# Optimization experiments

Measured on AMD Instinct MI355X. Metric: run time of the kernel, lower is better.

Reference implementation:

```python
import jax, jax.numpy as jnp
import numpy as np

B, T, D, H, E, M = 4, 2048, 2048, 8, 512, 8  # batch, seq, hidden, moe_heads, moe_experts, moe_dim//2
F = E * M  # flatten_shape = 4096
HALF = D // 2


def act(z):
    # 'relu2' activation: relu(x)**2
    r = jax.nn.relu(z)
    return r * r


def setup_inputs() -> dict:
    key = jax.random.key(0)
    ks = jax.random.split(key, 13)
    s = 0.02
    return {
        "x": jax.random.normal(ks[0], (B, T, D), jnp.float32),
        "g1": jax.random.uniform(ks[1], (B, T, H, E), jnp.float32),
        "g2": jax.random.uniform(ks[2], (B, T, H, E), jnp.float32),
        "u1_w": jax.random.normal(ks[3], (F, D), jnp.float32) * s,
        "u1_b": jnp.zeros((F,), jnp.float32),
        "u2_w": jax.random.normal(ks[4], (F, D), jnp.float32) * s,
        "u2_b": jnp.zeros((F,), jnp.float32),
        "v11_w": jax.random.normal(ks[5], (HALF, F), jnp.float32) * s,
        "v12_w": jax.random.normal(ks[6], (HALF, F), jnp.float32) * s,
        "v21_w": jax.random.normal(ks[7], (HALF, F), jnp.float32) * s,
        "v22_w": jax.random.normal(ks[8], (HALF, F), jnp.float32) * s,
        "b1": jax.random.normal(ks[9], (E, HALF), jnp.float32) * s,
        "b2": jax.random.normal(ks[10], (E, HALF), jnp.float32) * s,
    }


def reference(x, g1, g2, u1_w, u1_b, u2_w, u2_b, v11_w, v12_w, v21_w, v22_w, b1, b2):
    # x1, x2: [B,T,E,M]
    x1 = act(x @ u1_w.T + u1_b).reshape(B, T, E, M)
    x2 = act(x @ u2_w.T + u2_b).reshape(B, T, E, M)

    g1s = g1.sum(axis=2)  # [B,T,E] (einsum '...hi->...i')
    g2s = g2.sum(axis=2)

    # x11 = v11(einsum('btim,bthi->btim', x1, g1).flatten(-2))
    x11 = (x1 * g1s[..., None]).reshape(B, T, F) @ v11_w.T
    # x12 = v12(einsum('btjm,bthj,bthi->btim', x2, g2, g1).flatten(-2))
    t2 = jnp.einsum('btjm,bthj->bthm', x2, g2)
    x12 = jnp.einsum('bthm,bthi->btim', t2, g1).reshape(B, T, F) @ v12_w.T
    # x13 = einsum('bthi,id->btd', g1, b1)
    x13 = g1s @ b1

    # x21 = v21(einsum('btim,bthi,bthj->btjm', x1, g1, g2).flatten(-2))
    t1 = jnp.einsum('btim,bthi->bthm', x1, g1)
    x21 = jnp.einsum('bthm,bthj->btjm', t1, g2).reshape(B, T, F) @ v21_w.T
    # x22 = v22(einsum('btjm,bthj->btjm', x2, g2).flatten(-2))
    x22 = (x2 * g2s[..., None]).reshape(B, T, F) @ v22_w.T
    # x23 = einsum('bthj,jd->btd', g2, b2)
    x23 = g2s @ b2

    return jnp.concatenate((x11 + x12 + x13, x21 + x22 + x23), axis=-1)
```

## Files before the change

kernel.cpp:

```cpp
#include <hip/hip_runtime.h>
#include <hip/hip_bf16.h>

#define TOK   8192
#define DD    2048
#define FF    4096
#define EE    512
#define HALF  1024
#define KCAT  8704

typedef __bf16 bf16x8 __attribute__((ext_vector_type(8)));
typedef __bf16 bf16x4 __attribute__((ext_vector_type(4)));
typedef float  f32x4  __attribute__((ext_vector_type(4)));
using bf16 = __hip_bfloat16;

#define AS1(p) ((const __attribute__((address_space(1))) void*)(p))
#define AS3(p) ((__attribute__((address_space(3))) void*)(p))


__global__ void cvt_bf16(const float* __restrict__ in, bf16* __restrict__ out, int n4) {
    int i = blockIdx.x * blockDim.x + threadIdx.x;
    int stride = gridDim.x * blockDim.x;
    for (; i < n4; i += stride) {
        float4 v = ((const float4*)in)[i];
        bf16x4 o;
        o[0] = (__bf16)v.x; o[1] = (__bf16)v.y; o[2] = (__bf16)v.z; o[3] = (__bf16)v.w;
        ((bf16x4*)out)[i] = o;
    }
}

__global__ void pack_w(const float* __restrict__ vA, const float* __restrict__ vB,
                       const float* __restrict__ bmat, bf16* __restrict__ W) {
    int n = blockIdx.x;
    const float* ra = vA + (size_t)n * FF;
    const float* rb = vB + (size_t)n * FF;
    bf16* w = W + (size_t)n * KCAT;
    for (int k = threadIdx.x; k < FF; k += 256) {
        w[k]      = __float2bfloat16(ra[k]);
        w[FF + k] = __float2bfloat16(rb[k]);
    }
    for (int e = threadIdx.x; e < EE; e += 256)
        w[2 * FF + e] = __float2bfloat16(bmat[(size_t)e * HALF + n]);
}

template<int MODE>
__global__ __launch_bounds__(512, 2)
void gemm8(const bf16* __restrict__ A0, const bf16* __restrict__ B0,
           const float* __restrict__ bias0, void* __restrict__ C0,
           const bf16* __restrict__ A1, const bf16* __restrict__ B1,
           const float* __restrict__ bias1, void* __restrict__ C1,
           int nbm, int nbn, int K, int ldc)
{
    __shared__ __align__(16) char smem[3 * 32768];
    const int tid  = threadIdx.x;
    const int lane = tid & 63;
    const int wid  = tid >> 6;
    const int wm = wid >> 2, wn = wid & 3;
    const int r16 = lane & 15, kb = lane >> 4;

    int bid = blockIdx.x;
    {
        int nwg = gridDim.x;
        int q = nwg >> 3, r = nwg & 7;
        int xcd = bid & 7, idx = bid >> 3;
        bid = (xcd < r ? xcd * (q + 1) : r * (q + 1) + (xcd - r) * q) + idx;
    }
    const int npg = nbm * nbn;
    const int g   = bid / npg;
    const int lb  = bid - g * npg;
    const int bm = lb / nbn, bn = lb - bm * nbn;

    const bf16*  A    = g ? A1 : A0;
    const bf16*  Bw   = g ? B1 : B0;
    const float* bias = g ? bias1 : bias0;
    char* Cout = (char*)(g ? C1 : C0);

    const long row0 = (long)bm * 256;
    const int  col0 = bn * 256;
    const int  nt   = K >> 5;

    const char* gp[4];
    uint32_t ldst[4];
    #pragma unroll
    for (int l = 0; l < 4; ++l) {
        const int ab = l >> 1;
        const int li = l & 1;
        const uint32_t S = (uint32_t)(li * 512 + tid) * 16;
        const uint32_t L = S ^ (((S >> 7) & 3) << 4);
        const int r  = (int)(L >> 6);
        const int c2 = (int)(L & 63);
        const bf16* src = ab ? (Bw + (long)(col0 + r) * K) : (A + (row0 + r) * (long)K);
        gp[l]   = (const char*)src + c2;
        ldst[l] = (uint32_t)(ab * 16384) + (uint32_t)((li * 512 + (tid & ~63)) * 16);
    }

    uint32_t aoff, boff;
    {   int R0 = wm * 128 + r16;
        aoff = (uint32_t)((R0 * 64 + kb * 16) ^ (((R0 >> 1) & 3) << 4)); }
    {   int S0 = wn * 64 + r16;
        boff = 16384u + (uint32_t)((S0 * 64 + kb * 16) ^ (((S0 >> 1) & 3) << 4)); }

    f32x4 acc[8][4];
    #pragma unroll
    for (int i = 0; i < 8; ++i)
        #pragma unroll
        for (int j = 0; j < 4; ++j)
            acc[i][j] = (f32x4){0.f, 0.f, 0.f, 0.f};

    #pragma unroll
    for (int tt = 0; tt < 2; ++tt)
        #pragma unroll
        for (int l = 0; l < 4; ++l)
            __builtin_amdgcn_global_load_lds(AS1(gp[l] + tt * 64),
                                             AS3(smem + tt * 32768 + ldst[l]), 16, 0, 0);
    #pragma unroll
    for (int l = 0; l < 4; ++l) gp[l] += 128;

    int buf = 0;
    for (int t = 0; t < nt; ++t) {
        int sb = buf + 2; if (sb >= 3) sb -= 3;
        if (t + 2 < nt) {
            #pragma unroll
            for (int l = 0; l < 4; ++l) {
                __builtin_amdgcn_global_load_lds(AS1(gp[l]),
                                                 AS3(smem + sb * 32768 + ldst[l]), 16, 0, 0);
                gp[l] += 64;
            }
            asm volatile("s_waitcnt vmcnt(8)\n\ts_barrier" ::: "memory");
        } else if (t + 2 == nt) {
            asm volatile("s_waitcnt vmcnt(4)\n\ts_barrier" ::: "memory");
        } else {
            asm volatile("s_waitcnt vmcnt(0)\n\ts_barrier" ::: "memory");
        }

        const char* pb = smem + buf * 32768;
        bf16x8 af[8], bv[4];
        #pragma unroll
        for (int i = 0; i < 8; ++i)
            af[i] = *(const bf16x8*)(pb + aoff + i * 1024);
        #pragma unroll
        for (int j = 0; j < 4; ++j)
            bv[j] = *(const bf16x8*)(pb + boff + j * 1024);

        __builtin_amdgcn_s_setprio(1);
        #pragma unroll
        for (int i = 0; i < 8; ++i)
            #pragma unroll
            for (int j = 0; j < 4; ++j)
                acc[i][j] = __builtin_amdgcn_mfma_f32_16x16x32_bf16(af[i], bv[j], acc[i][j], 0, 0, 0);
        __builtin_amdgcn_s_setprio(0);

        asm volatile("s_barrier" ::: "memory");
        buf = (buf == 2) ? 0 : buf + 1;
    }

    const int rb = (lane >> 4) * 4;
    #pragma unroll
    for (int i = 0; i < 8; ++i) {
        #pragma unroll
        for (int j = 0; j < 4; ++j) {
            const int cc = col0 + wn * 64 + j * 16 + r16;
            float badd = 0.f;
            if (MODE == 1) badd = bias[cc];
            #pragma unroll
            for (int e = 0; e < 4; ++e) {
                long row = row0 + wm * 128 + i * 16 + rb + e;
                float v = acc[i][j][e];
                if (MODE == 1) {
                    v += badd;
                    v = fmaxf(v, 0.f);
                    v = v * v;
                    ((bf16*)Cout)[row * ldc + cc] = __float2bfloat16(v);
                } else {
                    ((float*)Cout)[row * ldc + cc] = v;
                }
            }
        }
    }
}

#define GPAD 524
__global__ __launch_bounds__(256)
void glue(const float* __restrict__ g1, const float* __restrict__ g2,
          bf16* __restrict__ Yl, bf16* __restrict__ Yr)
{
    __shared__ __align__(16) float g1t[8 * GPAD];
    __shared__ __align__(16) float g2t[8 * GPAD];
    __shared__ float g1s[EE], g2s[EE];
    __shared__ float t1s[64], t2s[64];
    __shared__ float t1p[4][64], t2p[4][64];
    __shared__ __align__(16) bf16 x1t[FF], x2t[FF];

    const int t   = blockIdx.x;
    const int tid = threadIdx.x;
    const float* g1p = g1 + (size_t)t * FF;
    const float* g2p = g2 + (size_t)t * FF;
    bf16* ylp = Yl + (size_t)t * KCAT;
    bf16* yrp = Yr + (size_t)t * KCAT;

    #pragma unroll
    for (int c = 0; c < 4; ++c) {
        int idx4 = (c * 256 + tid) * 4;
        float4 v1 = *(const float4*)(g1p + idx4);
        float4 v2 = *(const float4*)(g2p + idx4);
        int h = idx4 >> 9, e = idx4 & 511;
        *(float4*)&g1t[h * GPAD + e] = v1;
        *(float4*)&g2t[h * GPAD + e] = v2;
    }
    #pragma unroll
    for (int c = 0; c < 2; ++c) {
        int idx8 = (c * 256 + tid) * 8;
        *(bf16x8*)&x1t[idx8] = *(const bf16x8*)(ylp + idx8);
        *(bf16x8*)&x2t[idx8] = *(const bf16x8*)(yrp + FF + idx8);
    }
    __syncthreads();

    #pragma unroll
    for (int c = 0; c < 2; ++c) {
        int e = c * 256 + tid;
        float s1 = 0.f, s2 = 0.f;
        #pragma unroll
        for (int h = 0; h < 8; ++h) { s1 += g1t[h * GPAD + e]; s2 += g2t[h * GPAD + e]; }
        g1s[e] = s1; g2s[e] = s2;
    }

    {
        int o = tid & 63;
        int h = o & 7, m = o >> 3;
        int p = tid >> 6;
        float s1 = 0.f, s2 = 0.f;
        #pragma unroll 8
        for (int ii = 0; ii < 128; ++ii) {
            int e = p * 128 + ii;
            float xv1 = __bfloat162float(x1t[e * 8 + m]);
            float xv2 = __bfloat162float(x2t[e * 8 + m]);
            s1 += xv1 * g1t[h * GPAD + e];
            s2 += xv2 * g2t[h * GPAD + e];
        }
        t1p[p][o] = s1; t2p[p][o] = s2;
    }
    __syncthreads();
    if (tid < 64)       t1s[tid] = t1p[0][tid] + t1p[1][tid] + t1p[2][tid] + t1p[3][tid];
    else if (tid < 128) { int o = tid - 64; t2s[o] = t2p[0][o] + t2p[1][o] + t2p[2][o] + t2p[3][o]; }
    __syncthreads();

    #pragma unroll
    for (int c = 0; c < 2; ++c) {
        int f0 = (c * 256 + tid) * 8;
        int e  = f0 >> 3;
        float s1 = g1s[e], s2 = g2s[e];
        bf16x8 xa = *(const bf16x8*)&x1t[f0];
        bf16x8 xb = *(const bf16x8*)&x2t[f0];
        bf16x8 o1, o2;
        #pragma unroll
        for (int u = 0; u < 8; ++u) {
            o1[u] = (__bf16)((float)xa[u] * s1);
            o2[u] = (__bf16)((float)xb[u] * s2);
        }
        *(bf16x8*)(ylp + f0)      = o1;
        *(bf16x8*)(yrp + FF + f0) = o2;
    }
    #pragma unroll
    for (int c = 0; c < 2; ++c) {
        int f0 = (c * 256 + tid) * 8;
        int i  = f0 >> 3;
        bf16x8 o12v, o21v;
        #pragma unroll
        for (int m = 0; m < 8; ++m) {
            float s12 = 0.f, s21 = 0.f;
            #pragma unroll
            for (int h = 0; h < 8; ++h) {
                s12 += t2s[(m << 3) | h] * g1t[h * GPAD + i];
                s21 += t1s[(m << 3) | h] * g2t[h * GPAD + i];
            }
            o12v[m] = (__bf16)s12;
            o21v[m] = (__bf16)s21;
        }
        *(bf16x8*)(ylp + FF + f0) = o12v;
        *(bf16x8*)(yrp + f0)      = o21v;
    }
    {
        int e0 = tid * 2;
        ylp[2 * FF + e0]     = __float2bfloat16(g1s[e0]);
        ylp[2 * FF + e0 + 1] = __float2bfloat16(g1s[e0 + 1]);
        yrp[2 * FF + e0]     = __float2bfloat16(g2s[e0]);
        yrp[2 * FF + e0 + 1] = __float2bfloat16(g2s[e0 + 1]);
    }
}


extern "C" void kernel_launch(void* const* d_in, const int* in_sizes, int n_in,
                              void* d_out, int out_size, void* d_ws, size_t ws_size,
                              hipStream_t stream) {
    const float* x    = (const float*)d_in[0];
    const float* g1   = (const float*)d_in[1];
    const float* g2   = (const float*)d_in[2];
    const float* u1_w = (const float*)d_in[3];
    const float* u1_b = (const float*)d_in[4];
    const float* u2_w = (const float*)d_in[5];
    const float* u2_b = (const float*)d_in[6];
    const float* v11  = (const float*)d_in[7];
    const float* v12  = (const float*)d_in[8];
    const float* v21  = (const float*)d_in[9];
    const float* v22  = (const float*)d_in[10];
    const float* b1   = (const float*)d_in[11];
    const float* b2   = (const float*)d_in[12];
    float* out = (float*)d_out;

    size_t off = 0;
    char* base = (char*)d_ws;
    auto take = [&](size_t bytes) { void* p = base + off; off += (bytes + 255) & ~(size_t)255; return p; };
    bf16* Xb  = (bf16*)take((size_t)TOK * DD * 2);
    bf16* U1b = (bf16*)take((size_t)FF * DD * 2);
    bf16* U2b = (bf16*)take((size_t)FF * DD * 2);
    bf16* Wl  = (bf16*)take((size_t)HALF * KCAT * 2);
    bf16* Wr  = (bf16*)take((size_t)HALF * KCAT * 2);
    bf16* Yl  = (bf16*)take((size_t)TOK * KCAT * 2);
    bf16* Yr  = (bf16*)take((size_t)TOK * KCAT * 2);

    cvt_bf16<<<4096, 256, 0, stream>>>(x,    Xb,  TOK * DD / 4);
    cvt_bf16<<<2048, 256, 0, stream>>>(u1_w, U1b, FF * DD / 4);
    cvt_bf16<<<2048, 256, 0, stream>>>(u2_w, U2b, FF * DD / 4);
    pack_w<<<HALF, 256, 0, stream>>>(v11, v12, b1, Wl);
    pack_w<<<HALF, 256, 0, stream>>>(v21, v22, b2, Wr);

    gemm8<1><<<2 * (TOK / 256) * (FF / 256), 512, 0, stream>>>(
        Xb, U1b, u1_b, Yl,
        Xb, U2b, u2_b, Yr + FF,
        TOK / 256, FF / 256, DD, KCAT);

    glue<<<TOK, 256, 0, stream>>>(g1, g2, Yl, Yr);

    gemm8<0><<<2 * (TOK / 256) * (HALF / 256), 512, 0, stream>>>(
        Yl, Wl, nullptr, out,
        Yr, Wr, nullptr, out + HALF,
        TOK / 256, HALF / 256, KCAT, DD);
}
```

Baseline: 750.4 us.

## Rewrite GEMM mainloop with 32x32x16 MFMA and phased double-buffered 64-wide K tiles

Replaces the 16x16x32 MFMA GEMM with one that uses 32x32x16 MFMA tiles, a K step of 64 split into four phases, and a two-stage 128KB LDS double buffer. Global-to-LDS loads for the next tile are interleaved with the LDS reads and MFMAs of each phase, and the XOR swizzle is changed to match. The larger MFMA shape needs fewer LDS fragment reads per FLOP, and finer-grained phases are meant to hide load latency better. The cost is more barriers per iteration and 128KB of LDS per block, which may limit occupancy to one block per CU despite the launch bound of two.

Measured after the change: 831.0 us. +10.7%, slower.

```diff
diff --git a/kernel.cpp b/kernel.cpp
--- a/kernel.cpp
+++ b/kernel.cpp
@@ -11,6 +11,7 @@
 typedef __bf16 bf16x8 __attribute__((ext_vector_type(8)));
 typedef __bf16 bf16x4 __attribute__((ext_vector_type(4)));
 typedef float  f32x4  __attribute__((ext_vector_type(4)));
+typedef float  f32x16 __attribute__((ext_vector_type(16)));
 using bf16 = __hip_bfloat16;
 
 #define AS1(p) ((const __attribute__((address_space(1))) void*)(p))
@@ -44,18 +45,18 @@
 
 template<int MODE>
 __global__ __launch_bounds__(512, 2)
-void gemm8(const bf16* __restrict__ A0, const bf16* __restrict__ B0,
-           const float* __restrict__ bias0, void* __restrict__ C0,
-           const bf16* __restrict__ A1, const bf16* __restrict__ B1,
-           const float* __restrict__ bias1, void* __restrict__ C1,
-           int nbm, int nbn, int K, int ldc)
+void gemm32(const bf16* __restrict__ A0, const bf16* __restrict__ B0,
+            const float* __restrict__ bias0, void* __restrict__ C0,
+            const bf16* __restrict__ A1, const bf16* __restrict__ B1,
+            const float* __restrict__ bias1, void* __restrict__ C1,
+            int nbm, int nbn, int K, int ldc)
 {
-    __shared__ __align__(16) char smem[3 * 32768];
+    __shared__ __align__(16) char smem[131072];
     const int tid  = threadIdx.x;
     const int lane = tid & 63;
     const int wid  = tid >> 6;
     const int wm = wid >> 2, wn = wid & 3;
-    const int r16 = lane & 15, kb = lane >> 4;
+    const int ln31 = lane & 31, kb = lane >> 5;
 
     int bid = blockIdx.x;
     {
@@ -76,95 +77,110 @@
 
     const long row0 = (long)bm * 256;
     const int  col0 = bn * 256;
-    const int  nt   = K >> 5;
-
-    const char* gp[4];
-    uint32_t ldst[4];
-    #pragma unroll
-    for (int l = 0; l < 4; ++l) {
-        const int ab = l >> 1;
-        const int li = l & 1;
-        const uint32_t S = (uint32_t)(li * 512 + tid) * 16;
-        const uint32_t L = S ^ (((S >> 7) & 3) << 4);
-        const int r  = (int)(L >> 6);
-        const int c2 = (int)(L & 63);
-        const bf16* src = ab ? (Bw + (long)(col0 + r) * K) : (A + (row0 + r) * (long)K);
-        gp[l]   = (const char*)src + c2;
-        ldst[l] = (uint32_t)(ab * 16384) + (uint32_t)((li * 512 + (tid & ~63)) * 16);
-    }
-
-    uint32_t aoff, boff;
-    {   int R0 = wm * 128 + r16;
-        aoff = (uint32_t)((R0 * 64 + kb * 16) ^ (((R0 >> 1) & 3) << 4)); }
-    {   int S0 = wn * 64 + r16;
-        boff = 16384u + (uint32_t)((S0 * 64 + kb * 16) ^ (((S0 >> 1) & 3) << 4)); }
-
-    f32x4 acc[8][4];
-    #pragma unroll
-    for (int i = 0; i < 8; ++i)
-        #pragma unroll
-        for (int j = 0; j < 4; ++j)
-            acc[i][j] = (f32x4){0.f, 0.f, 0.f, 0.f};
-
-    #pragma unroll
-    for (int tt = 0; tt < 2; ++tt)
-        #pragma unroll
-        for (int l = 0; l < 4; ++l)
-            __builtin_amdgcn_global_load_lds(AS1(gp[l] + tt * 64),
-                                             AS3(smem + tt * 32768 + ldst[l]), 16, 0, 0);
-    #pragma unroll
-    for (int l = 0; l < 4; ++l) gp[l] += 128;
-
-    int buf = 0;
+    const int  nt   = K >> 6;
+
+    const char* gA[2]; const char* gB[2];
+    uint32_t ldst0, ldst1;
+    #pragma unroll
+    for (int l = 0; l < 2; ++l) {
+        const uint32_t S = (uint32_t)(l * 512 + tid) * 16;
+        const int r  = (int)(S >> 6);
+        const int cb = (int)((S & 63) ^ ((uint32_t)(r & 3) << 4));
+        gA[l] = (const char*)A + (row0 + r) * (long)K * 2 + cb;
+        gB[l] = (const char*)Bw + (long)(col0 + r) * K * 2 + cb;
+    }
+    ldst0 = (uint32_t)(tid & ~63) * 16;
+    ldst1 = 8192u + (uint32_t)(tid & ~63) * 16;
+
+    const uint32_t aB = (uint32_t)(wm * 128 + ln31) * 64;
+    const uint32_t bB = 32768u + (uint32_t)(wn * 64 + ln31) * 64;
+    const uint32_t coffE = (uint32_t)((kb ^ (lane & 3)) << 4);
+    const uint32_t coffO = (uint32_t)(((kb | 2) ^ (lane & 3)) << 4);
+
+    f32x16 acc[4][2];
+    #pragma unroll
+    for (int i = 0; i < 4; ++i)
+        #pragma unroll
+        for (int j = 0; j < 2; ++j)
+            acc[i][j] = (f32x16)(0.f);
+
+    __builtin_amdgcn_global_load_lds(AS1(gA[0]),      AS3(smem +     0 + ldst0), 16, 0, 0);
+    __builtin_amdgcn_global_load_lds(AS1(gA[1]),      AS3(smem +     0 + ldst1), 16, 0, 0);
+    __builtin_amdgcn_global_load_lds(AS1(gB[0]),      AS3(smem + 32768 + ldst0), 16, 0, 0);
+    __builtin_amdgcn_global_load_lds(AS1(gB[1]),      AS3(smem + 32768 + ldst1), 16, 0, 0);
+    __builtin_amdgcn_global_load_lds(AS1(gA[0] + 64), AS3(smem + 16384 + ldst0), 16, 0, 0);
+    __builtin_amdgcn_global_load_lds(AS1(gA[1] + 64), AS3(smem + 16384 + ldst1), 16, 0, 0);
+    __builtin_amdgcn_global_load_lds(AS1(gB[0] + 64), AS3(smem + 49152 + ldst0), 16, 0, 0);
+    __builtin_amdgcn_global_load_lds(AS1(gB[1] + 64), AS3(smem + 49152 + ldst1), 16, 0, 0);
+    asm volatile("s_waitcnt vmcnt(4)\n\ts_barrier" ::: "memory");
+
+#define MFMA8()                                                                        \
+    __builtin_amdgcn_s_setprio(1);                                                     \
+    acc[0][0] = __builtin_amdgcn_mfma_f32_32x32x16_bf16(a0, b0, acc[0][0], 0, 0, 0);   \
+    acc[0][1] = __builtin_amdgcn_mfma_f32_32x32x16_bf16(a0, b1, acc[0][1], 0, 0, 0);   \
+    acc[1][0] = __builtin_amdgcn_mfma_f32_32x32x16_bf16(a1, b0, acc[1][0], 0, 0, 0);   \
+    acc[1][1] = __builtin_amdgcn_mfma_f32_32x32x16_bf16(a1, b1, acc[1][1], 0, 0, 0);   \
+    acc[2][0] = __builtin_amdgcn_mfma_f32_32x32x16_bf16(a2, b0, acc[2][0], 0, 0, 0);   \
+    acc[2][1] = __builtin_amdgcn_mfma_f32_32x32x16_bf16(a2, b1, acc[2][1], 0, 0, 0);   \
+    acc[3][0] = __builtin_amdgcn_mfma_f32_32x32x16_bf16(a3, b0, acc[3][0], 0, 0, 0);   \
+    acc[3][1] = __builtin_amdgcn_mfma_f32_32x32x16_bf16(a3, b1, acc[3][1], 0, 0, 0);   \
+    __builtin_amdgcn_s_setprio(0);
+
+#define PHASE(Q, LOFF, COFFv)                                                          \
+    {                                                                                  \
+        if (st) {                                                                      \
+            __builtin_amdgcn_global_load_lds(                                          \
+                AS1(((Q & 1) ? gB : gA)[0] + koff + (Q >> 1) * 64),                    \
+                AS3(pt + LOFF + ldst0), 16, 0, 0);                                     \
+            __builtin_amdgcn_global_load_lds(                                          \
+                AS1(((Q & 1) ? gB : gA)[1] + koff + (Q >> 1) * 64),                    \
+                AS3(pt + LOFF + ldst1), 16, 0, 0);                                     \
+        }                                                                              \
+        const char* ps = pb + (Q >> 1) * 16384;                                        \
+        bf16x8 a0 = *(const bf16x8*)(ps + aB + COFFv);                                 \
+        bf16x8 a1 = *(const bf16x8*)(ps + aB + 2048 + COFFv);                          \
+        bf16x8 a2 = *(const bf16x8*)(ps + aB + 4096 + COFFv);                          \
+        bf16x8 a3 = *(const bf16x8*)(ps + aB + 6144 + COFFv);                          \
+        bf16x8 b0 = *(const bf16x8*)(ps + bB + COFFv);                                 \
+        bf16x8 b1 = *(const bf16x8*)(ps + bB + 2048 + COFFv);                          \
+        asm volatile("s_barrier" ::: "memory");                                        \
+        MFMA8();                                                                       \
+    }
+
     for (int t = 0; t < nt; ++t) {
-        int sb = buf + 2; if (sb >= 3) sb -= 3;
-        if (t + 2 < nt) {
-            #pragma unroll
-            for (int l = 0; l < 4; ++l) {
-                __builtin_amdgcn_global_load_lds(AS1(gp[l]),
-                                                 AS3(smem + sb * 32768 + ldst[l]), 16, 0, 0);
-                gp[l] += 64;
-            }
-            asm volatile("s_waitcnt vmcnt(8)\n\ts_barrier" ::: "memory");
-        } else if (t + 2 == nt) {
-            asm volatile("s_waitcnt vmcnt(4)\n\ts_barrier" ::: "memory");
-        } else {
-            asm volatile("s_waitcnt vmcnt(0)\n\ts_barrier" ::: "memory");
-        }
-
-        const char* pb = smem + buf * 32768;
-        bf16x8 af[8], bv[4];
-        #pragma unroll
-        for (int i = 0; i < 8; ++i)
-            af[i] = *(const bf16x8*)(pb + aoff + i * 1024);
-        #pragma unroll
-        for (int j = 0; j < 4; ++j)
-            bv[j] = *(const bf16x8*)(pb + boff + j * 1024);
-
-        __builtin_amdgcn_s_setprio(1);
-        #pragma unroll
-        for (int i = 0; i < 8; ++i)
-            #pragma unroll
-            for (int j = 0; j < 4; ++j)
-                acc[i][j] = __builtin_amdgcn_mfma_f32_16x16x32_bf16(af[i], bv[j], acc[i][j], 0, 0, 0);
-        __builtin_amdgcn_s_setprio(0);
-
+        char* pb = smem + (t & 1) * 65536;
+        char* pt = smem + ((t + 1) & 1) * 65536;
+        const bool st = (t + 1 < nt);
+        const long koff = (long)(t + 1) * 128;
+
+        PHASE(0, 0, coffE)
         asm volatile("s_barrier" ::: "memory");
-        buf = (buf == 2) ? 0 : buf + 1;
-    }
-
-    const int rb = (lane >> 4) * 4;
-    #pragma unroll
-    for (int i = 0; i < 8; ++i) {
-        #pragma unroll
-        for (int j = 0; j < 4; ++j) {
-            const int cc = col0 + wn * 64 + j * 16 + r16;
+        PHASE(1, 32768, coffO)
+        if (st) asm volatile("s_waitcnt vmcnt(4)" ::: "memory");
+        else    asm volatile("s_waitcnt vmcnt(0)" ::: "memory");
+        asm volatile("s_barrier" ::: "memory");
+        PHASE(2, 16384, coffE)
+        asm volatile("s_barrier" ::: "memory");
+        PHASE(3, 49152, coffO)
+        if (st) asm volatile("s_waitcnt vmcnt(4)" ::: "memory");
+        asm volatile("s_barrier" ::: "memory");
+    }
+#undef PHASE
+#undef MFMA8
+
+    const int rowb = wm * 128 + kb * 4;
+    const int colb = col0 + wn * 64 + ln31;
+    #pragma unroll
+    for (int i = 0; i < 4; ++i) {
+        #pragma unroll
+        for (int j = 0; j < 2; ++j) {
+            const int cc = colb + j * 32;
             float badd = 0.f;
             if (MODE == 1) badd = bias[cc];
             #pragma unroll
-            for (int e = 0; e < 4; ++e) {
-                long row = row0 + wm * 128 + i * 16 + rb + e;
-                float v = acc[i][j][e];
+            for (int rg = 0; rg < 16; ++rg) {
+                long row = row0 + rowb + i * 32 + (rg & 3) + 8 * (rg >> 2);
+                float v = acc[i][j][rg];
                 if (MODE == 1) {
                     v += badd;
                     v = fmaxf(v, 0.f);
@@ -323,14 +339,14 @@
     pack_w<<<HALF, 256, 0, stream>>>(v11, v12, b1, Wl);
     pack_w<<<HALF, 256, 0, stream>>>(v21, v22, b2, Wr);
 
-    gemm8<1><<<2 * (TOK / 256) * (FF / 256), 512, 0, stream>>>(
+    gemm32<1><<<2 * (TOK / 256) * (FF / 256), 512, 0, stream>>>(
         Xb, U1b, u1_b, Yl,
         Xb, U2b, u2_b, Yr + FF,
         TOK / 256, FF / 256, DD, KCAT);
 
     glue<<<TOK, 256, 0, stream>>>(g1, g2, Yl, Yr);
 
-    gemm8<0><<<2 * (TOK / 256) * (HALF / 256), 512, 0, stream>>>(
+    gemm32<0><<<2 * (TOK / 256) * (HALF / 256), 512, 0, stream>>>(
         Yl, Wl, nullptr, out,
         Yr, Wr, nullptr, out + HALF,
         TOK / 256, HALF / 256, KCAT, DD);
```

## Restructure GEMM mainloop into ping-pong pipeline with K=64 tiles and split MFMA phases

Applied to the files above, without the earlier changes.

Replaces the triple-buffered K=32 mainloop with a double-buffered K=64 tile (128KB LDS) and splits each iteration into four MFMA phases. Each phase interleaves a quarter of the next tile's global-to-LDS loads with LDS fragment reads, separated by barriers. The intent is to overlap memory traffic with MFMA work at finer granularity and to cut per-tile loop overhead. The larger LDS footprint may allow only one 512-thread block per CU despite launch_bounds(512,2), and the extra barriers add synchronisation cost.

Result: faster. 714.4 us (-4.8%).

```diff
diff --git a/kernel.cpp b/kernel.cpp
--- a/kernel.cpp
+++ b/kernel.cpp
@@ -44,13 +44,13 @@
 
 template<int MODE>
 __global__ __launch_bounds__(512, 2)
-void gemm8(const bf16* __restrict__ A0, const bf16* __restrict__ B0,
+void gemmP(const bf16* __restrict__ A0, const bf16* __restrict__ B0,
            const float* __restrict__ bias0, void* __restrict__ C0,
            const bf16* __restrict__ A1, const bf16* __restrict__ B1,
            const float* __restrict__ bias1, void* __restrict__ C1,
            int nbm, int nbn, int K, int ldc)
 {
-    __shared__ __align__(16) char smem[3 * 32768];
+    __shared__ __align__(16) char smem[131072];
     const int tid  = threadIdx.x;
     const int lane = tid & 63;
     const int wid  = tid >> 6;
@@ -76,28 +76,22 @@
 
     const long row0 = (long)bm * 256;
     const int  col0 = bn * 256;
-    const int  nt   = K >> 5;
-
-    const char* gp[4];
-    uint32_t ldst[4];
-    #pragma unroll
-    for (int l = 0; l < 4; ++l) {
-        const int ab = l >> 1;
-        const int li = l & 1;
-        const uint32_t S = (uint32_t)(li * 512 + tid) * 16;
-        const uint32_t L = S ^ (((S >> 7) & 3) << 4);
-        const int r  = (int)(L >> 6);
-        const int c2 = (int)(L & 63);
-        const bf16* src = ab ? (Bw + (long)(col0 + r) * K) : (A + (row0 + r) * (long)K);
-        gp[l]   = (const char*)src + c2;
-        ldst[l] = (uint32_t)(ab * 16384) + (uint32_t)((li * 512 + (tid & ~63)) * 16);
-    }
-
-    uint32_t aoff, boff;
-    {   int R0 = wm * 128 + r16;
-        aoff = (uint32_t)((R0 * 64 + kb * 16) ^ (((R0 >> 1) & 3) << 4)); }
-    {   int S0 = wn * 64 + r16;
-        boff = 16384u + (uint32_t)((S0 * 64 + kb * 16) ^ (((S0 >> 1) & 3) << 4)); }
+    const int  nt   = K >> 6;
+
+    const char* gA[2]; const char* gB[2];
+    #pragma unroll
+    for (int l = 0; l < 2; ++l) {
+        const uint32_t S = (uint32_t)(l * 512 + tid) * 16;
+        const int r  = (int)(S >> 6);
+        const int cb = (int)((S & 63) ^ ((uint32_t)((r >> 1) & 3) << 4));
+        gA[l] = (const char*)A  + (row0 + r) * (long)K * 2 + cb;
+        gB[l] = (const char*)Bw + (long)(col0 + r) * K * 2 + cb;
+    }
+    const uint32_t ldst = (uint32_t)(tid & ~63) * 16;
+
+    const uint32_t swz  = ((uint32_t)(r16 >> 1) & 3u) << 4;
+    const uint32_t aoff = (uint32_t)((wm * 128 + r16) * 64 + kb * 16) ^ swz;
+    const uint32_t boff = (uint32_t)((wn * 64  + r16) * 64 + kb * 16) ^ swz;
 
     f32x4 acc[8][4];
     #pragma unroll
@@ -106,52 +100,84 @@
         for (int j = 0; j < 4; ++j)
             acc[i][j] = (f32x4){0.f, 0.f, 0.f, 0.f};
 
-    #pragma unroll
-    for (int tt = 0; tt < 2; ++tt)
-        #pragma unroll
-        for (int l = 0; l < 4; ++l)
-            __builtin_amdgcn_global_load_lds(AS1(gp[l] + tt * 64),
-                                             AS3(smem + tt * 32768 + ldst[l]), 16, 0, 0);
-    #pragma unroll
-    for (int l = 0; l < 4; ++l) gp[l] += 128;
-
-    int buf = 0;
+    __builtin_amdgcn_global_load_lds(AS1(gA[0]),      AS3(smem +     0 + ldst), 16, 0, 0);
+    __builtin_amdgcn_global_load_lds(AS1(gA[1]),      AS3(smem +  8192 + ldst), 16, 0, 0);
+    __builtin_amdgcn_global_load_lds(AS1(gB[0]),      AS3(smem + 32768 + ldst), 16, 0, 0);
+    __builtin_amdgcn_global_load_lds(AS1(gB[1]),      AS3(smem + 40960 + ldst), 16, 0, 0);
+    __builtin_amdgcn_global_load_lds(AS1(gA[0] + 64), AS3(smem + 16384 + ldst), 16, 0, 0);
+    __builtin_amdgcn_global_load_lds(AS1(gA[1] + 64), AS3(smem + 24576 + ldst), 16, 0, 0);
+    __builtin_amdgcn_global_load_lds(AS1(gB[0] + 64), AS3(smem + 49152 + ldst), 16, 0, 0);
+    __builtin_amdgcn_global_load_lds(AS1(gB[1] + 64), AS3(smem + 57344 + ldst), 16, 0, 0);
+    asm volatile("s_waitcnt vmcnt(4)\n\ts_barrier" ::: "memory");
+
+#define MFMA16(IH)                                                                       \
+    __builtin_amdgcn_s_setprio(1);                                                      \
+    _Pragma("unroll")                                                                    \
+    for (int fi = 0; fi < 4; ++fi) {                                                     \
+        acc[(IH)*4+fi][0] = __builtin_amdgcn_mfma_f32_16x16x32_bf16(af[fi], bv[0], acc[(IH)*4+fi][0], 0, 0, 0); \
+        acc[(IH)*4+fi][1] = __builtin_amdgcn_mfma_f32_16x16x32_bf16(af[fi], bv[1], acc[(IH)*4+fi][1], 0, 0, 0); \
+        acc[(IH)*4+fi][2] = __builtin_amdgcn_mfma_f32_16x16x32_bf16(af[fi], bv[2], acc[(IH)*4+fi][2], 0, 0, 0); \
+        acc[(IH)*4+fi][3] = __builtin_amdgcn_mfma_f32_16x16x32_bf16(af[fi], bv[3], acc[(IH)*4+fi][3], 0, 0, 0); \
+    }                                                                                    \
+    __builtin_amdgcn_s_setprio(0);
+
     for (int t = 0; t < nt; ++t) {
-        int sb = buf + 2; if (sb >= 3) sb -= 3;
-        if (t + 2 < nt) {
-            #pragma unroll
-            for (int l = 0; l < 4; ++l) {
-                __builtin_amdgcn_global_load_lds(AS1(gp[l]),
-                                                 AS3(smem + sb * 32768 + ldst[l]), 16, 0, 0);
-                gp[l] += 64;
-            }
-            asm volatile("s_waitcnt vmcnt(8)\n\ts_barrier" ::: "memory");
-        } else if (t + 2 == nt) {
-            asm volatile("s_waitcnt vmcnt(4)\n\ts_barrier" ::: "memory");
+        const char* pb = smem + (t & 1) * 65536;
+        char*       pt = smem + ((t + 1) & 1) * 65536;
+        const bool  st = (t + 1 < nt);
+        const long  koff = (long)(t + 1) * 128;
+
+        bf16x8 af[4], bv[4];
+
+        #pragma unroll
+        for (int fj = 0; fj < 4; ++fj) bv[fj] = *(const bf16x8*)(pb + 32768 + boff + fj * 1024);
+        #pragma unroll
+        for (int fi = 0; fi < 4; ++fi) af[fi] = *(const bf16x8*)(pb + aoff + fi * 1024);
+        if (st) {
+            __builtin_amdgcn_global_load_lds(AS1(gA[0] + koff), AS3(pt +    0 + ldst), 16, 0, 0);
+            __builtin_amdgcn_global_load_lds(AS1(gA[1] + koff), AS3(pt + 8192 + ldst), 16, 0, 0);
+        }
+        asm volatile("s_barrier" ::: "memory");
+        MFMA16(0)
+        asm volatile("s_barrier" ::: "memory");
+
+        #pragma unroll
+        for (int fi = 0; fi < 4; ++fi) af[fi] = *(const bf16x8*)(pb + 4096 + aoff + fi * 1024);
+        if (st) {
+            __builtin_amdgcn_global_load_lds(AS1(gB[0] + koff), AS3(pt + 32768 + ldst), 16, 0, 0);
+            __builtin_amdgcn_global_load_lds(AS1(gB[1] + koff), AS3(pt + 40960 + ldst), 16, 0, 0);
+            asm volatile("s_waitcnt vmcnt(4)" ::: "memory");
         } else {
-            asm volatile("s_waitcnt vmcnt(0)\n\ts_barrier" ::: "memory");
-        }
-
-        const char* pb = smem + buf * 32768;
-        bf16x8 af[8], bv[4];
-        #pragma unroll
-        for (int i = 0; i < 8; ++i)
-            af[i] = *(const bf16x8*)(pb + aoff + i * 1024);
-        #pragma unroll
-        for (int j = 0; j < 4; ++j)
-            bv[j] = *(const bf16x8*)(pb + boff + j * 1024);
-
-        __builtin_amdgcn_s_setprio(1);
-        #pragma unroll
-        for (int i = 0; i < 8; ++i)
-            #pragma unroll
-            for (int j = 0; j < 4; ++j)
-                acc[i][j] = __builtin_amdgcn_mfma_f32_16x16x32_bf16(af[i], bv[j], acc[i][j], 0, 0, 0);
-        __builtin_amdgcn_s_setprio(0);
-
-        asm volatile("s_barrier" ::: "memory");
-        buf = (buf == 2) ? 0 : buf + 1;
-    }
+            asm volatile("s_waitcnt vmcnt(0)" ::: "memory");
+        }
+        asm volatile("s_barrier" ::: "memory");
+        MFMA16(1)
+        asm volatile("s_barrier" ::: "memory");
+
+        #pragma unroll
+        for (int fj = 0; fj < 4; ++fj) bv[fj] = *(const bf16x8*)(pb + 49152 + boff + fj * 1024);
+        #pragma unroll
+        for (int fi = 0; fi < 4; ++fi) af[fi] = *(const bf16x8*)(pb + 16384 + aoff + fi * 1024);
+        if (st) {
+            __builtin_amdgcn_global_load_lds(AS1(gA[0] + koff + 64), AS3(pt + 16384 + ldst), 16, 0, 0);
+            __builtin_amdgcn_global_load_lds(AS1(gA[1] + koff + 64), AS3(pt + 24576 + ldst), 16, 0, 0);
+        }
+        asm volatile("s_barrier" ::: "memory");
+        MFMA16(0)
+        asm volatile("s_barrier" ::: "memory");
+
+        #pragma unroll
+        for (int fi = 0; fi < 4; ++fi) af[fi] = *(const bf16x8*)(pb + 16384 + 4096 + aoff + fi * 1024);
+        if (st) {
+            __builtin_amdgcn_global_load_lds(AS1(gB[0] + koff + 64), AS3(pt + 49152 + ldst), 16, 0, 0);
+            __builtin_amdgcn_global_load_lds(AS1(gB[1] + koff + 64), AS3(pt + 57344 + ldst), 16, 0, 0);
+            asm volatile("s_waitcnt vmcnt(4)" ::: "memory");
+        }
+        asm volatile("s_barrier" ::: "memory");
+        MFMA16(1)
+        asm volatile("s_barrier" ::: "memory");
+    }
+#undef MFMA16
 
     const int rb = (lane >> 4) * 4;
     #pragma unroll
@@ -323,14 +349,14 @@
     pack_w<<<HALF, 256, 0, stream>>>(v11, v12, b1, Wl);
     pack_w<<<HALF, 256, 0, stream>>>(v21, v22, b2, Wr);
 
-    gemm8<1><<<2 * (TOK / 256) * (FF / 256), 512, 0, stream>>>(
+    gemmP<1><<<2 * (TOK / 256) * (FF / 256), 512, 0, stream>>>(
         Xb, U1b, u1_b, Yl,
         Xb, U2b, u2_b, Yr + FF,
         TOK / 256, FF / 256, DD, KCAT);
 
     glue<<<TOK, 256, 0, stream>>>(g1, g2, Yl, Yr);
 
-    gemm8<0><<<2 * (TOK / 256) * (HALF / 256), 512, 0, stream>>>(
+    gemmP<0><<<2 * (TOK / 256) * (HALF / 256), 512, 0, stream>>>(
         Yl, Wl, nullptr, out,
         Yr, Wr, nullptr, out + HALF,
         TOK / 256, HALF / 256, KCAT, DD);
```
